# Performance work log

Measured on AMD Instinct MI355X. Metric: run time of the kernel, lower is better.

Reference implementation:

```python
import jax, jax.numpy as jnp
import numpy as np

N = 200_000   # nodes in batched graph
E = 400_000   # edges
D = 128       # embed_dim
L = 5         # num_layer
G = 1000      # number of graphs in batch
ATOM_V = 119  # atom vocab (OGB)
BOND_V = 5    # bond vocab (OGB)
OUT = 128     # output_dim
EPS = 1e-5


def setup_inputs() -> dict:
    key = jax.random.key(0)
    ks = jax.random.split(key, 16)
    inp = {
        "nfeat": jax.random.randint(ks[0], (N,), 0, ATOM_V),
        "efeat": jax.random.randint(ks[1], (E,), 0, BOND_V),
        "src": jax.random.randint(ks[2], (E,), 0, N),
        "dst": jax.random.randint(ks[3], (E,), 0, N),
        "node2graph": jnp.sort(jax.random.randint(ks[4], (N,), 0, G)),
        # learned parameters
        "atom_emb": jax.random.normal(ks[5], (ATOM_V, D), jnp.float32) * 0.02,
        "edge_emb": jax.random.normal(ks[6], (L, BOND_V, D), jnp.float32) * 0.02,
        "W": jax.random.normal(ks[7], (L, D, D), jnp.float32) * 0.02,
        "b": jnp.zeros((L, D), jnp.float32),
        "gamma": jnp.ones((L, D), jnp.float32),
        "beta": jnp.zeros((L, D), jnp.float32),
        "W1": jax.random.normal(ks[8], (D, D), jnp.float32) * 0.02,
        "b1": jnp.zeros((D,), jnp.float32),
        "W2": jax.random.normal(ks[9], (D, OUT), jnp.float32) * 0.02,
        "b2": jnp.zeros((OUT,), jnp.float32),
    }
    return inp


def reference(nfeat, efeat, src, dst, node2graph,
              atom_emb, edge_emb, W, b, gamma, beta, W1, b1, W2, b2):
    h = atom_emb[nfeat]                                  # [N, D]
    # in-degree + 1 (GCNConvLayer degree norm)
    deg = jax.ops.segment_sum(jnp.ones((E,), h.dtype), dst, num_segments=N) + 1.0
    for l in range(L):
        e = edge_emb[l][efeat]                           # [E, D] edge encoder
        m = h[src] + e                                   # u_add_e
        neigh = jax.ops.segment_sum(m, dst, num_segments=N)  # fn.sum -> 'neigh'
        h = ((h + neigh) / deg[:, None]) @ W[l] + b[l]   # project_node_feat
        # batch norm over nodes (training-mode batch stats), affine
        mu = jnp.mean(h, axis=0)
        var = jnp.var(h, axis=0)
        h = (h - mu) * jax.lax.rsqrt(var + EPS) * gamma[l] + beta[l]
        h = jax.nn.relu(h)                               # activation; dropout=eval
    # global mean pooling per graph
    cnt = jax.ops.segment_sum(jnp.ones((N,), h.dtype), node2graph, num_segments=G)
    g = jax.ops.segment_sum(h, node2graph, num_segments=G) / jnp.maximum(cnt, 1.0)[:, None]
    # predict MLP (dropout in eval mode = identity)
    out = jax.nn.relu(g @ W1 + b1) @ W2 + b2             # [G, OUT]
    return out
```

## Files before the change

kernel.cpp:

```cpp
#include <hip/hip_runtime.h>
#include <hip/hip_bf16.h>
#include <cstddef>

#define NN 200000
#define NE 400000
#define DD 128
#define NL 5
#define NG 1000
#define BOND_V 5
#define BM 32
#define NBLK (NN / BM)
#define MAXD 16
#define CHUNK 100
#define NB_SCAN 200
#define CH 1000
#define SB 125
#define EPS 1e-5f
#define XS 136

typedef __bf16 bf16x8 __attribute__((ext_vector_type(8)));
typedef float floatx4 __attribute__((ext_vector_type(4)));

__device__ __forceinline__ unsigned short f2bf(float f) {
    unsigned int u = __float_as_uint(f);
    u = (u + 0x7fffu + ((u >> 16) & 1u)) >> 16;
    return (unsigned short)u;
}
__device__ __forceinline__ float bf2f(unsigned short s) {
    return __uint_as_float(((unsigned int)s) << 16);
}
__device__ __forceinline__ float4 bf4_to_f4(uint2 v) {
    float4 o;
    o.x = __uint_as_float(v.x << 16);
    o.y = __uint_as_float(v.x & 0xffff0000u);
    o.z = __uint_as_float(v.y << 16);
    o.w = __uint_as_float(v.y & 0xffff0000u);
    return o;
}
__device__ __forceinline__ float4 actv4(float4 h, float4 sc, float4 sh) {
    float4 o;
    o.x = fmaxf(0.f, h.x * sc.x + sh.x);
    o.y = fmaxf(0.f, h.y * sc.y + sh.y);
    o.z = fmaxf(0.f, h.z * sc.z + sh.z);
    o.w = fmaxf(0.f, h.w * sc.w + sh.w);
    return o;
}

__global__ void k_setup1(const int* __restrict__ dst, int* __restrict__ cnt,
                         const int* __restrict__ n2g, float* __restrict__ gcnt,
                         const float* __restrict__ W, unsigned short* __restrict__ Wht,
                         unsigned short* __restrict__ Wlt) {
    int e = blockIdx.x * blockDim.x + threadIdx.x;
    if (e < NE) atomicAdd(&cnt[dst[e]], 1);
    if (e < NN) atomicAdd(&gcnt[n2g[e]], 1.0f);
    if (e < NL * DD * DD) {
        int l = e / (DD * DD), rem = e % (DD * DD);
        int k = rem / DD, n = rem % DD;
        float v = W[e];
        unsigned short hb = f2bf(v);
        unsigned short lb = f2bf(v - bf2f(hb));
        size_t o = (size_t)l * DD * DD + (size_t)n * DD + k;
        Wht[o] = hb; Wlt[o] = lb;
    }
}

__global__ void k_scan1(const int* __restrict__ cnt, int* __restrict__ bsum) {
    __shared__ int sh[256];
    int b = blockIdx.x, t = threadIdx.x;
    int s = 0;
    if (t < CH / 4) {
        int base = b * CH + t * 4;
        s = cnt[base] + cnt[base + 1] + cnt[base + 2] + cnt[base + 3];
    }
    sh[t] = s;
    __syncthreads();
    if (t == 0) {
        int tot = 0;
        for (int i = 0; i < CH / 4; i++) tot += sh[i];
        bsum[b] = tot;
    }
}

__global__ void k_scan2(const int* __restrict__ bsum, int* __restrict__ bpre,
                        int* __restrict__ off) {
    if (threadIdx.x == 0) {
        int run = 0;
        for (int i = 0; i < NB_SCAN; i++) { bpre[i] = run; run += bsum[i]; }
        off[NN] = NE;
    }
}

__global__ void k_scan3(const int* __restrict__ cnt, const int* __restrict__ bpre,
                        int* __restrict__ off, int* __restrict__ cur,
                        float* __restrict__ rdeg) {
    __shared__ int sh[256];
    int b = blockIdx.x, t = threadIdx.x;
    int base = b * CH + t * 4;
    int c0 = 0, c1 = 0, c2 = 0, c3 = 0, s = 0;
    if (t < CH / 4) {
        c0 = cnt[base]; c1 = cnt[base + 1]; c2 = cnt[base + 2]; c3 = cnt[base + 3];
        s = c0 + c1 + c2 + c3;
    }
    sh[t] = s;
    __syncthreads();
    if (t == 0) {
        int run = bpre[b];
        for (int i = 0; i < CH / 4; i++) { int v = sh[i]; sh[i] = run; run += v; }
    }
    __syncthreads();
    if (t < CH / 4) {
        int run = sh[t];
        off[base] = run; cur[base] = run; run += c0;
        off[base + 1] = run; cur[base + 1] = run; run += c1;
        off[base + 2] = run; cur[base + 2] = run; run += c2;
        off[base + 3] = run; cur[base + 3] = run;
        rdeg[base]     = 1.0f / (float)(c0 + 1);
        rdeg[base + 1] = 1.0f / (float)(c1 + 1);
        rdeg[base + 2] = 1.0f / (float)(c2 + 1);
        rdeg[base + 3] = 1.0f / (float)(c3 + 1);
    }
}

__global__ void k_bucket(const int* __restrict__ src, const int* __restrict__ dst,
                         const int* __restrict__ efeat, int* __restrict__ cur,
                         int* __restrict__ esrc, int* __restrict__ eft) {
    int e = blockIdx.x * blockDim.x + threadIdx.x;
    if (e < NE) {
        int p = atomicAdd(&cur[dst[e]], 1);
        esrc[p] = src[e];
        eft[p] = efeat[e];
    }
}

__global__ void k_pad(const int* __restrict__ off, const int* __restrict__ esrc,
                      const int* __restrict__ eft, const int* __restrict__ nfeat,
                      int* __restrict__ pent, int* __restrict__ pent0,
                      int* __restrict__ bperm, int* __restrict__ gmax) {
    __shared__ int offL[BM + 1];
    __shared__ int degS[BM];
    __shared__ int sortIdx[BM];
    __shared__ int gmaxS[8];
    int b = blockIdx.x, tid = threadIdx.x;
    if (tid <= BM) offL[tid] = off[b * BM + tid];
    __syncthreads();
    if (tid < BM) degS[tid] = offL[tid + 1] - offL[tid];
    __syncthreads();
    if (tid < BM) {
        int d = degS[tid], rank = 0;
        #pragma unroll
        for (int j = 0; j < BM; j++)
            rank += (degS[j] > d) || (degS[j] == d && j < tid);
        sortIdx[rank] = tid;
    }
    __syncthreads();
    if (tid < 8) {
        int g = degS[sortIdx[tid * 4]];
        gmaxS[tid] = g;
        gmax[b * 8 + tid] = g;
    }
    if (tid < BM) bperm[b * BM + tid] = sortIdx[tid];
    __syncthreads();
    for (int idx = tid; idx < BM * MAXD; idx += 256) {
        int p = idx & 31, j = idx >> 5, g = p >> 2;
        int gm = gmaxS[g]; if (gm > MAXD) gm = MAXD;
        if (j < gm) {
            int row = sortIdx[p];
            int d = degS[row];
            int v, v0;
            if (j < d) {
                int e = offL[row] + j;
                int s = esrc[e], f = eft[e];
                v = s | (f << 18);
                v0 = nfeat[s] | (f << 18);
            } else { v = (5 << 18); v0 = (5 << 18); }
            pent[(size_t)b * MAXD * BM + j * BM + p] = v;
            pent0[(size_t)b * MAXD * BM + j * BM + p] = v0;
        }
    }
}

__global__ __launch_bounds__(256, 4)
void k_fused(const void* __restrict__ basep, const int* __restrict__ nfeat, int first,
             const int* __restrict__ off, const int* __restrict__ esrc,
             const int* __restrict__ eft, const int* __restrict__ pentsel,
             const int* __restrict__ bperm, const int* __restrict__ gmax,
             const float* __restrict__ eemb, const float* __restrict__ rdeg,
             const float* __restrict__ scP, const float* __restrict__ shP,
             const unsigned short* __restrict__ Wht, const unsigned short* __restrict__ Wlt,
             const float* __restrict__ bias,
             unsigned short* __restrict__ C, float* __restrict__ part) {
    __shared__ unsigned short Xh[BM * XS];
    __shared__ unsigned short Xl[BM * XS];
    __shared__ float eSr[6 * DD];
    __shared__ int pentL[BM * MAXD];
    __shared__ int offL[BM + 1];
    __shared__ int permL[BM];
    __shared__ int gmL[8];

    const float* baseF = (const float*)basep;
    const unsigned short* baseB = (const unsigned short*)basep;

    int tid = threadIdx.x;
    int n0 = blockIdx.x * BM;
    if (tid < 160) *(float4*)(eSr + tid * 4) = *(const float4*)(eemb + tid * 4);
    else if (tid < 192) *(float4*)(eSr + tid * 4) = (float4){0.f, 0.f, 0.f, 0.f};
    if (tid <= BM) offL[tid] = off[n0 + tid];
    if (tid < BM) permL[tid] = bperm[blockIdx.x * BM + tid];
    if (tid < 8) gmL[tid] = gmax[blockIdx.x * 8 + tid];
    {
        const int2* pg = (const int2*)(pentsel + (size_t)blockIdx.x * MAXD * BM);
        *(int2*)(pentL + tid * 2) = pg[tid];
    }

    int lane32 = tid & 31, grp = tid >> 5;
    int c4 = lane32 << 2;
    float4 sc4, sh4;
    if (!first) {
        sc4 = *(const float4*)(scP + c4);
        sh4 = *(const float4*)(shP + c4);
    }
    __syncthreads();

    int rows[4];
    #pragma unroll
    for (int i = 0; i < 4; i++) rows[i] = permL[grp * 4 + i];

    float4 acc[4];
    #pragma unroll
    for (int i = 0; i < 4; i++) {
        int n = n0 + rows[i];
        if (first) {
            acc[i] = *(const float4*)(baseF + (size_t)nfeat[n] * DD + c4);
        } else {
            uint2 g = *(const uint2*)(baseB + (size_t)n * DD + c4);
            acc[i] = actv4(bf4_to_f4(g), sc4, sh4);
        }
    }

    int gmx = gmL[grp];
    int jmax = gmx < MAXD ? gmx : MAXD;
    const int* pL = pentL + grp * 4;
    int j = 0;
    if (first) {
        for (; j + 2 <= jmax; j += 2) {
            int a0 = pL[j*32+0], a1 = pL[j*32+1], a2 = pL[j*32+2], a3 = pL[j*32+3];
            int b0 = pL[j*32+32], b1 = pL[j*32+33], b2 = pL[j*32+34], b3 = pL[j*32+35];
            float4 ha0 = *(const float4*)(baseF + (size_t)(a0 & 0x3FFFF) * DD + c4);
            float4 ha1 = *(const float4*)(baseF + (size_t)(a1 & 0x3FFFF) * DD + c4);
            float4 ha2 = *(const float4*)(baseF + (size_t)(a2 & 0x3FFFF) * DD + c4);
            float4 ha3 = *(const float4*)(baseF + (size_t)(a3 & 0x3FFFF) * DD + c4);
            float4 hb0 = *(const float4*)(baseF + (size_t)(b0 & 0x3FFFF) * DD + c4);
            float4 hb1 = *(const float4*)(baseF + (size_t)(b1 & 0x3FFFF) * DD + c4);
            float4 hb2 = *(const float4*)(baseF + (size_t)(b2 & 0x3FFFF) * DD + c4);
            float4 hb3 = *(const float4*)(baseF + (size_t)(b3 & 0x3FFFF) * DD + c4);
            int fa0 = a0 >> 18, fa1 = a1 >> 18, fa2 = a2 >> 18, fa3 = a3 >> 18;
            int fb0 = b0 >> 18, fb1 = b1 >> 18, fb2 = b2 >> 18, fb3 = b3 >> 18;
            float wa0 = (fa0 == 5) ? 0.f : 1.f, wa1 = (fa1 == 5) ? 0.f : 1.f;
            float wa2 = (fa2 == 5) ? 0.f : 1.f, wa3 = (fa3 == 5) ? 0.f : 1.f;
            float wb0 = (fb0 == 5) ? 0.f : 1.f, wb1 = (fb1 == 5) ? 0.f : 1.f;
            float wb2 = (fb2 == 5) ? 0.f : 1.f, wb3 = (fb3 == 5) ? 0.f : 1.f;
            float4 ea0 = *(const float4*)(eSr + fa0 * DD + c4);
            float4 ea1 = *(const float4*)(eSr + fa1 * DD + c4);
            float4 ea2 = *(const float4*)(eSr + fa2 * DD + c4);
            float4 ea3 = *(const float4*)(eSr + fa3 * DD + c4);
            float4 eb0 = *(const float4*)(eSr + fb0 * DD + c4);
            float4 eb1 = *(const float4*)(eSr + fb1 * DD + c4);
            float4 eb2 = *(const float4*)(eSr + fb2 * DD + c4);
            float4 eb3 = *(const float4*)(eSr + fb3 * DD + c4);
            acc[0].x += (ha0.x + ea0.x) * wa0 + (hb0.x + eb0.x) * wb0;
            acc[0].y += (ha0.y + ea0.y) * wa0 + (hb0.y + eb0.y) * wb0;
            acc[0].z += (ha0.z + ea0.z) * wa0 + (hb0.z + eb0.z) * wb0;
            acc[0].w += (ha0.w + ea0.w) * wa0 + (hb0.w + eb0.w) * wb0;
            acc[1].x += (ha1.x + ea1.x) * wa1 + (hb1.x + eb1.x) * wb1;
            acc[1].y += (ha1.y + ea1.y) * wa1 + (hb1.y + eb1.y) * wb1;
            acc[1].z += (ha1.z + ea1.z) * wa1 + (hb1.z + eb1.z) * wb1;
            acc[1].w += (ha1.w + ea1.w) * wa1 + (hb1.w + eb1.w) * wb1;
            acc[2].x += (ha2.x + ea2.x) * wa2 + (hb2.x + eb2.x) * wb2;
            acc[2].y += (ha2.y + ea2.y) * wa2 + (hb2.y + eb2.y) * wb2;
            acc[2].z += (ha2.z + ea2.z) * wa2 + (hb2.z + eb2.z) * wb2;
            acc[2].w += (ha2.w + ea2.w) * wa2 + (hb2.w + eb2.w) * wb2;
            acc[3].x += (ha3.x + ea3.x) * wa3 + (hb3.x + eb3.x) * wb3;
            acc[3].y += (ha3.y + ea3.y) * wa3 + (hb3.y + eb3.y) * wb3;
            acc[3].z += (ha3.z + ea3.z) * wa3 + (hb3.z + eb3.z) * wb3;
            acc[3].w += (ha3.w + ea3.w) * wa3 + (hb3.w + eb3.w) * wb3;
        }
        for (; j < jmax; j++) {
            int a0 = pL[j*32+0], a1 = pL[j*32+1], a2 = pL[j*32+2], a3 = pL[j*32+3];
            float4 h0 = *(const float4*)(baseF + (size_t)(a0 & 0x3FFFF) * DD + c4);
            float4 h1 = *(const float4*)(baseF + (size_t)(a1 & 0x3FFFF) * DD + c4);
            float4 h2 = *(const float4*)(baseF + (size_t)(a2 & 0x3FFFF) * DD + c4);
            float4 h3 = *(const float4*)(baseF + (size_t)(a3 & 0x3FFFF) * DD + c4);
            int f0 = a0 >> 18, f1 = a1 >> 18, f2 = a2 >> 18, f3 = a3 >> 18;
            float w0 = (f0 == 5) ? 0.f : 1.f, w1 = (f1 == 5) ? 0.f : 1.f;
            float w2 = (f2 == 5) ? 0.f : 1.f, w3 = (f3 == 5) ? 0.f : 1.f;
            float4 e0 = *(const float4*)(eSr + f0 * DD + c4);
            float4 e1 = *(const float4*)(eSr + f1 * DD + c4);
            float4 e2 = *(const float4*)(eSr + f2 * DD + c4);
            float4 e3 = *(const float4*)(eSr + f3 * DD + c4);
            acc[0].x += (h0.x + e0.x) * w0; acc[0].y += (h0.y + e0.y) * w0;
            acc[0].z += (h0.z + e0.z) * w0; acc[0].w += (h0.w + e0.w) * w0;
            acc[1].x += (h1.x + e1.x) * w1; acc[1].y += (h1.y + e1.y) * w1;
            acc[1].z += (h1.z + e1.z) * w1; acc[1].w += (h1.w + e1.w) * w1;
            acc[2].x += (h2.x + e2.x) * w2; acc[2].y += (h2.y + e2.y) * w2;
            acc[2].z += (h2.z + e2.z) * w2; acc[2].w += (h2.w + e2.w) * w2;
            acc[3].x += (h3.x + e3.x) * w3; acc[3].y += (h3.y + e3.y) * w3;
            acc[3].z += (h3.z + e3.z) * w3; acc[3].w += (h3.w + e3.w) * w3;
        }
    } else {
        for (; j + 2 <= jmax; j += 2) {
            int a0 = pL[j*32+0], a1 = pL[j*32+1], a2 = pL[j*32+2], a3 = pL[j*32+3];
            int b0 = pL[j*32+32], b1 = pL[j*32+33], b2 = pL[j*32+34], b3 = pL[j*32+35];
            uint2 ga0 = *(const uint2*)(baseB + (size_t)(a0 & 0x3FFFF) * DD + c4);
            uint2 ga1 = *(const uint2*)(baseB + (size_t)(a1 & 0x3FFFF) * DD + c4);
            uint2 ga2 = *(const uint2*)(baseB + (size_t)(a2 & 0x3FFFF) * DD + c4);
            uint2 ga3 = *(const uint2*)(baseB + (size_t)(a3 & 0x3FFFF) * DD + c4);
            uint2 gb0 = *(const uint2*)(baseB + (size_t)(b0 & 0x3FFFF) * DD + c4);
            uint2 gb1 = *(const uint2*)(baseB + (size_t)(b1 & 0x3FFFF) * DD + c4);
            uint2 gb2 = *(const uint2*)(baseB + (size_t)(b2 & 0x3FFFF) * DD + c4);
            uint2 gb3 = *(const uint2*)(baseB + (size_t)(b3 & 0x3FFFF) * DD + c4);
            float4 ha0 = actv4(bf4_to_f4(ga0), sc4, sh4);
            float4 ha1 = actv4(bf4_to_f4(ga1), sc4, sh4);
            float4 ha2 = actv4(bf4_to_f4(ga2), sc4, sh4);
            float4 ha3 = actv4(bf4_to_f4(ga3), sc4, sh4);
            float4 hb0 = actv4(bf4_to_f4(gb0), sc4, sh4);
            float4 hb1 = actv4(bf4_to_f4(gb1), sc4, sh4);
            float4 hb2 = actv4(bf4_to_f4(gb2), sc4, sh4);
            float4 hb3 = actv4(bf4_to_f4(gb3), sc4, sh4);
            int fa0 = a0 >> 18, fa1 = a1 >> 18, fa2 = a2 >> 18, fa3 = a3 >> 18;
            int fb0 = b0 >> 18, fb1 = b1 >> 18, fb2 = b2 >> 18, fb3 = b3 >> 18;
            float wa0 = (fa0 == 5) ? 0.f : 1.f, wa1 = (fa1 == 5) ? 0.f : 1.f;
            float wa2 = (fa2 == 5) ? 0.f : 1.f, wa3 = (fa3 == 5) ? 0.f : 1.f;
            float wb0 = (fb0 == 5) ? 0.f : 1.f, wb1 = (fb1 == 5) ? 0.f : 1.f;
            float wb2 = (fb2 == 5) ? 0.f : 1.f, wb3 = (fb3 == 5) ? 0.f : 1.f;
            float4 ea0 = *(const float4*)(eSr + fa0 * DD + c4);
            float4 ea1 = *(const float4*)(eSr + fa1 * DD + c4);
            float4 ea2 = *(const float4*)(eSr + fa2 * DD + c4);
            float4 ea3 = *(const float4*)(eSr + fa3 * DD + c4);
            float4 eb0 = *(const float4*)(eSr + fb0 * DD + c4);
            float4 eb1 = *(const float4*)(eSr + fb1 * DD + c4);
            float4 eb2 = *(const float4*)(eSr + fb2 * DD + c4);
            float4 eb3 = *(const float4*)(eSr + fb3 * DD + c4);
            acc[0].x += (ha0.x + ea0.x) * wa0 + (hb0.x + eb0.x) * wb0;
            acc[0].y += (ha0.y + ea0.y) * wa0 + (hb0.y + eb0.y) * wb0;
            acc[0].z += (ha0.z + ea0.z) * wa0 + (hb0.z + eb0.z) * wb0;
            acc[0].w += (ha0.w + ea0.w) * wa0 + (hb0.w + eb0.w) * wb0;
            acc[1].x += (ha1.x + ea1.x) * wa1 + (hb1.x + eb1.x) * wb1;
            acc[1].y += (ha1.y + ea1.y) * wa1 + (hb1.y + eb1.y) * wb1;
            acc[1].z += (ha1.z + ea1.z) * wa1 + (hb1.z + eb1.z) * wb1;
            acc[1].w += (ha1.w + ea1.w) * wa1 + (hb1.w + eb1.w) * wb1;
            acc[2].x += (ha2.x + ea2.x) * wa2 + (hb2.x + eb2.x) * wb2;
            acc[2].y += (ha2.y + ea2.y) * wa2 + (hb2.y + eb2.y) * wb2;
            acc[2].z += (ha2.z + ea2.z) * wa2 + (hb2.z + eb2.z) * wb2;
            acc[2].w += (ha2.w + ea2.w) * wa2 + (hb2.w + eb2.w) * wb2;
            acc[3].x += (ha3.x + ea3.x) * wa3 + (hb3.x + eb3.x) * wb3;
            acc[3].y += (ha3.y + ea3.y) * wa3 + (hb3.y + eb3.y) * wb3;
            acc[3].z += (ha3.z + ea3.z) * wa3 + (hb3.z + eb3.z) * wb3;
            acc[3].w += (ha3.w + ea3.w) * wa3 + (hb3.w + eb3.w) * wb3;
        }
        for (; j < jmax; j++) {
            int a0 = pL[j*32+0], a1 = pL[j*32+1], a2 = pL[j*32+2], a3 = pL[j*32+3];
            uint2 g0 = *(const uint2*)(baseB + (size_t)(a0 & 0x3FFFF) * DD + c4);
            uint2 g1 = *(const uint2*)(baseB + (size_t)(a1 & 0x3FFFF) * DD + c4);
            uint2 g2 = *(const uint2*)(baseB + (size_t)(a2 & 0x3FFFF) * DD + c4);
            uint2 g3 = *(const uint2*)(baseB + (size_t)(a3 & 0x3FFFF) * DD + c4);
            float4 h0 = actv4(bf4_to_f4(g0), sc4, sh4);
            float4 h1 = actv4(bf4_to_f4(g1), sc4, sh4);
            float4 h2 = actv4(bf4_to_f4(g2), sc4, sh4);
            float4 h3 = actv4(bf4_to_f4(g3), sc4, sh4);
            int f0 = a0 >> 18, f1 = a1 >> 18, f2 = a2 >> 18, f3 = a3 >> 18;
            float w0 = (f0 == 5) ? 0.f : 1.f, w1 = (f1 == 5) ? 0.f : 1.f;
            float w2 = (f2 == 5) ? 0.f : 1.f, w3 = (f3 == 5) ? 0.f : 1.f;
            float4 e0 = *(const float4*)(eSr + f0 * DD + c4);
            float4 e1 = *(const float4*)(eSr + f1 * DD + c4);
            float4 e2 = *(const float4*)(eSr + f2 * DD + c4);
            float4 e3 = *(const float4*)(eSr + f3 * DD + c4);
            acc[0].x += (h0.x + e0.x) * w0; acc[0].y += (h0.y + e0.y) * w0;
            acc[0].z += (h0.z + e0.z) * w0; acc[0].w += (h0.w + e0.w) * w0;
            acc[1].x += (h1.x + e1.x) * w1; acc[1].y += (h1.y + e1.y) * w1;
            acc[1].z += (h1.z + e1.z) * w1; acc[1].w += (h1.w + e1.w) * w1;
            acc[2].x += (h2.x + e2.x) * w2; acc[2].y += (h2.y + e2.y) * w2;
            acc[2].z += (h2.z + e2.z) * w2; acc[2].w += (h2.w + e2.w) * w2;
            acc[3].x += (h3.x + e3.x) * w3; acc[3].y += (h3.y + e3.y) * w3;
            acc[3].z += (h3.z + e3.z) * w3; acc[3].w += (h3.w + e3.w) * w3;
        }
    }

    if (gmx > MAXD) {
        #pragma unroll
        for (int i = 0; i < 4; i++) {
            int row = rows[i];
            for (int e = offL[row] + MAXD; e < offL[row + 1]; e++) {
                int s = esrc[e], f = eft[e];
                float4 hv;
                if (first) {
                    hv = *(const float4*)(baseF + (size_t)nfeat[s] * DD + c4);
                } else {
                    uint2 g = *(const uint2*)(baseB + (size_t)s * DD + c4);
                    hv = actv4(bf4_to_f4(g), sc4, sh4);
                }
                const float* ep = eSr + f * DD + c4;
                acc[i].x += hv.x + ep[0]; acc[i].y += hv.y + ep[1];
                acc[i].z += hv.z + ep[2]; acc[i].w += hv.w + ep[3];
            }
        }
    }

    #pragma unroll
    for (int i = 0; i < 4; i++) {
        int r = rows[i];
        float rd = rdeg[n0 + r];
        float ax = acc[i].x * rd, ay = acc[i].y * rd, az = acc[i].z * rd, aw = acc[i].w * rd;
        unsigned short h0 = f2bf(ax), h1 = f2bf(ay), h2 = f2bf(az), h3 = f2bf(aw);
        unsigned short l0 = f2bf(ax - bf2f(h0));
        unsigned short l1 = f2bf(ay - bf2f(h1));
        unsigned short l2 = f2bf(az - bf2f(h2));
        unsigned short l3 = f2bf(aw - bf2f(h3));
        uint2 hv2, lv2;
        hv2.x = (unsigned)h0 | ((unsigned)h1 << 16);
        hv2.y = (unsigned)h2 | ((unsigned)h3 << 16);
        lv2.x = (unsigned)l0 | ((unsigned)l1 << 16);
        lv2.y = (unsigned)l2 | ((unsigned)l3 << 16);
        *(uint2*)(Xh + r * XS + c4) = hv2;
        *(uint2*)(Xl + r * XS + c4) = lv2;
    }
    __syncthreads();

    int lane = tid & 63, w = tid >> 6;
    int m16 = lane & 15, quad = lane >> 4;
    int rowTile = w & 1;
    int colBase = (w >> 1) << 6;
    int rowA = rowTile * 16 + m16;

    floatx4 acc4[4];
    #pragma unroll
    for (int t = 0; t < 4; t++) acc4[t] = (floatx4){0.f, 0.f, 0.f, 0.f};

    #pragma unroll
    for (int kp = 0; kp < 4; kp++) {
        bf16x8 ah = *(const bf16x8*)(Xh + rowA * XS + kp * 32 + quad * 8);
        bf16x8 al = *(const bf16x8*)(Xl + rowA * XS + kp * 32 + quad * 8);
        #pragma unroll
        for (int t = 0; t < 4; t++) {
            int ncol = colBase + t * 16 + m16;
            bf16x8 bh = *(const bf16x8*)(Wht + (size_t)ncol * DD + kp * 32 + quad * 8);
            bf16x8 bl = *(const bf16x8*)(Wlt + (size_t)ncol * DD + kp * 32 + quad * 8);
            acc4[t] = __builtin_amdgcn_mfma_f32_16x16x32_bf16(ah, bh, acc4[t], 0, 0, 0);
            acc4[t] = __builtin_amdgcn_mfma_f32_16x16x32_bf16(ah, bl, acc4[t], 0, 0, 0);
            acc4[t] = __builtin_amdgcn_mfma_f32_16x16x32_bf16(al, bh, acc4[t], 0, 0, 0);
        }
    }
    __syncthreads();

    float* redS = eSr;
    float* redQ = eSr + 2 * DD;
    unsigned short* Cs = Xh;
    #pragma unroll
    for (int t = 0; t < 4; t++) {
        int col = colBase + t * 16 + m16;
        float bv = bias[col];
        float s = 0.f, q = 0.f;
        #pragma unroll
        for (int rr = 0; rr < 4; rr++) {
            float vv = acc4[t][rr] + bv;
            s += vv; q += vv * vv;
            Cs[(rowTile * 16 + quad * 4 + rr) * XS + col] = f2bf(vv);
        }
        s += __shfl_xor(s, 16); q += __shfl_xor(q, 16);
        s += __shfl_xor(s, 32); q += __shfl_xor(q, 32);
        if (lane < 16) { redS[rowTile * DD + col] = s; redQ[rowTile * DD + col] = q; }
    }
    __syncthreads();

    #pragma unroll
    for (int it = 0; it < 2; it++) {
        int idx = it * 256 + tid;
        int row = idx >> 4, q16 = idx & 15;
        uint4 v = *(const uint4*)(Cs + row * XS + q16 * 8);
        *(uint4*)(C + (size_t)(n0 + row) * DD + q16 * 8) = v;
    }
    if (tid < DD) {
        float ss = redS[tid] + redS[DD + tid];
        float qq = redQ[tid] + redQ[DD + tid];
        part[(size_t)blockIdx.x * 256 + tid] = ss;
        part[(size_t)blockIdx.x * 256 + DD + tid] = qq;
    }
}

__global__ void k_stats(const float* __restrict__ part, float* __restrict__ acc,
                        int* __restrict__ cnt,
                        const float* __restrict__ gamma, const float* __restrict__ beta,
                        float* __restrict__ scale, float* __restrict__ shift) {
    int t = threadIdx.x;
    float s = 0.f;
    int base = blockIdx.x * (NBLK / SB);
    for (int i = 0; i < NBLK / SB; i++)
        s += part[(size_t)(base + i) * 256 + t];
    atomicAdd(&acc[t], s);
    __threadfence();
    __shared__ int lastS;
    __syncthreads();
    if (t == 0) lastS = (atomicAdd(cnt, 1) == SB - 1);
    __syncthreads();
    if (lastS && t < DD) {
        float Sv = atomicAdd(&acc[t], 0.0f);
        float Qv = atomicAdd(&acc[DD + t], 0.0f);
        float m = Sv / (float)NN;
        float v = Qv / (float)NN - m * m;
        float rs = rsqrtf(v + EPS);
        float sc = rs * gamma[t];
        scale[t] = sc;
        shift[t] = beta[t] - m * sc;
    }
}

__global__ void k_bnpool(const unsigned short* __restrict__ A, const int* __restrict__ n2g,
                         const float* __restrict__ scale, const float* __restrict__ shift,
                         float* __restrict__ gsum) {
    int j = threadIdx.x;
    int n0 = blockIdx.x * CHUNK;
    float sc = scale[j], sh = shift[j];
    int cur = n2g[n0];
    float acc = 0.f;
    for (int i = 0; i < CHUNK; i++) {
        int n = n0 + i;
        int gg = n2g[n];
        if (gg != cur) {
            atomicAdd(&gsum[(size_t)cur * DD + j], acc);
            acc = 0.f;
            cur = gg;
        }
        float x = bf2f(A[(size_t)n * DD + j]);
        acc += fmaxf(0.f, x * sc + sh);
    }
    atomicAdd(&gsum[(size_t)cur * DD + j], acc);
}

__global__ void k_mlp(const float* __restrict__ gsum, const float* __restrict__ gcnt,
                      const float* __restrict__ W1, const float* __restrict__ b1,
                      const float* __restrict__ W2, const float* __restrict__ b2,
                      float* __restrict__ out) {
    __shared__ float gs[DD], hs[DD];
    int gid = blockIdx.x, j = threadIdx.x;
    float inv = 1.0f / fmaxf(gcnt[gid], 1.0f);
    gs[j] = gsum[(size_t)gid * DD + j] * inv;
    __syncthreads();
    float a = b1[j];
    for (int k = 0; k < DD; k++) a += gs[k] * W1[k * DD + j];
    hs[j] = fmaxf(a, 0.f);
    __syncthreads();
    float o = b2[j];
    for (int k = 0; k < DD; k++) o += hs[k] * W2[k * DD + j];
    out[(size_t)gid * DD + j] = o;
}

extern "C" void kernel_launch(void* const* d_in, const int* in_sizes, int n_in,
                              void* d_out, int out_size, void* d_ws, size_t ws_size,
                              hipStream_t stream) {
    const int*   nfeat = (const int*)d_in[0];
    const int*   efeat = (const int*)d_in[1];
    const int*   src   = (const int*)d_in[2];
    const int*   dst   = (const int*)d_in[3];
    const int*   n2g   = (const int*)d_in[4];
    const float* aemb  = (const float*)d_in[5];
    const float* eemb  = (const float*)d_in[6];
    const float* Wl    = (const float*)d_in[7];
    const float* bl    = (const float*)d_in[8];
    const float* gam   = (const float*)d_in[9];
    const float* bet   = (const float*)d_in[10];
    const float* W1    = (const float*)d_in[11];
    const float* b1    = (const float*)d_in[12];
    const float* W2    = (const float*)d_in[13];
    const float* b2    = (const float*)d_in[14];
    float* out = (float*)d_out;

    unsigned short* H0 = (unsigned short*)d_ws;
    unsigned short* H1 = H0 + (size_t)NN * DD;
    float* rdeg   = (float*)(H1 + (size_t)NN * DD);
    float* gsum   = rdeg + NN;
    float* gcnt   = gsum + (size_t)NG * DD;
    float* scaleA = gcnt + NG;
    float* shiftA = scaleA + NL * DD;
    float* accS   = shiftA + NL * DD;
    int*   scnt   = (int*)(accS + NL * 256);
    float* part   = (float*)(scnt + 16);
    unsigned short* Wht = (unsigned short*)(part + (size_t)NBLK * 256);
    unsigned short* Wlt = Wht + (size_t)NL * DD * DD;
    int* off   = (int*)(Wlt + (size_t)NL * DD * DD);
    int* cur   = off + NN + 1;
    int* esrc  = cur + NN;
    int* eft   = esrc + NE;
    int* cnt   = eft + NE;
    int* bsum  = cnt + NN;
    int* bpre  = bsum + NB_SCAN;
    int* bperm = bpre + NB_SCAN;
    int* gmax  = bperm + (size_t)NBLK * BM;
    int* pent  = gmax + (size_t)NBLK * 8;
    int* pent0 = pent + (size_t)NBLK * MAXD * BM;

    hipMemsetAsync(gsum, 0, (size_t)(NG * DD + NG) * sizeof(float), stream);
    hipMemsetAsync(accS, 0, (size_t)(NL * 256) * sizeof(float) + 16 * sizeof(int), stream);
    hipMemsetAsync(cnt, 0, (size_t)NN * sizeof(int), stream);

    k_setup1<<<(NE + 255) / 256, 256, 0, stream>>>(dst, cnt, n2g, gcnt, Wl, Wht, Wlt);
    k_scan1<<<NB_SCAN, 256, 0, stream>>>(cnt, bsum);
    k_scan2<<<1, 64, 0, stream>>>(bsum, bpre, off);
    k_scan3<<<NB_SCAN, 256, 0, stream>>>(cnt, bpre, off, cur, rdeg);
    k_bucket<<<(NE + 255) / 256, 256, 0, stream>>>(src, dst, efeat, cur, esrc, eft);
    k_pad<<<NBLK, 256, 0, stream>>>(off, esrc, eft, nfeat, pent, pent0, bperm, gmax);

    unsigned short* hcur = H0;
    for (int l = 0; l < NL; l++) {
        const void* base = (l == 0) ? (const void*)aemb : (const void*)hcur;
        unsigned short* hnext = (l == 0) ? H0 : ((hcur == H0) ? H1 : H0);
        const int* psel = (l == 0) ? pent0 : pent;
        const float* scP = scaleA + (size_t)((l == 0) ? 0 : (l - 1)) * DD;
        const float* shP = shiftA + (size_t)((l == 0) ? 0 : (l - 1)) * DD;
        k_fused<<<NBLK, 256, 0, stream>>>(base, nfeat, (l == 0) ? 1 : 0,
                                          off, esrc, eft, psel, bperm, gmax,
                                          eemb + (size_t)l * BOND_V * DD, rdeg,
                                          scP, shP,
                                          Wht + (size_t)l * DD * DD,
                                          Wlt + (size_t)l * DD * DD,
                                          bl + (size_t)l * DD, hnext, part);
        k_stats<<<SB, 256, 0, stream>>>(part, accS + l * 256, scnt + l,
                                        gam + (size_t)l * DD, bet + (size_t)l * DD,
                                        scaleA + (size_t)l * DD, shiftA + (size_t)l * DD);
        hcur = hnext;
    }
    k_bnpool<<<NN / CHUNK, DD, 0, stream>>>(hcur, n2g,
                                            scaleA + (size_t)(NL - 1) * DD,
                                            shiftA + (size_t)(NL - 1) * DD, gsum);
    k_mlp<<<NG, DD, 0, stream>>>(gsum, gcnt, W1, b1, W2, b2, out);
}
```

Measured before the change: 1.036 ms.

## Software-pipeline neighbor gathers, drop smem metadata, vectorize pooling kernel

In the layered aggregation kernel, the non-first path now prefetches the next edge slot's neighbor rows while accumulating the current ones (unroll-1 double buffer). Per-block metadata (perm, gmax, offsets) is read straight from global memory instead of staged through shared memory, and the barrier is moved after the self-row loads. k_pad always fills all MAXD padded slots so the kernel can round the trip count up to even without a remainder loop. Launch bounds are raised to 6 waves per EU, and the pooling kernel uses 256 threads with bf16x4 vector loads over 8 node stripes. The cost is extra padded iterations, possible register pressure at the higher occupancy target, and more atomics in pooling.

```diff
diff --git a/kernel.cpp b/kernel.cpp
--- a/kernel.cpp
+++ b/kernel.cpp
@@ -11,7 +11,7 @@
 #define BM 32
 #define NBLK (NN / BM)
 #define MAXD 16
-#define CHUNK 100
+#define PCH 200
 #define NB_SCAN 200
 #define CH 1000
 #define SB 125
@@ -139,7 +139,6 @@
     __shared__ int offL[BM + 1];
     __shared__ int degS[BM];
     __shared__ int sortIdx[BM];
-    __shared__ int gmaxS[8];
     int b = blockIdx.x, tid = threadIdx.x;
     if (tid <= BM) offL[tid] = off[b * BM + tid];
     __syncthreads();
@@ -153,33 +152,26 @@
         sortIdx[rank] = tid;
     }
     __syncthreads();
-    if (tid < 8) {
-        int g = degS[sortIdx[tid * 4]];
-        gmaxS[tid] = g;
-        gmax[b * 8 + tid] = g;
-    }
+    if (tid < 8) gmax[b * 8 + tid] = degS[sortIdx[tid * 4]];
     if (tid < BM) bperm[b * BM + tid] = sortIdx[tid];
     __syncthreads();
     for (int idx = tid; idx < BM * MAXD; idx += 256) {
-        int p = idx & 31, j = idx >> 5, g = p >> 2;
-        int gm = gmaxS[g]; if (gm > MAXD) gm = MAXD;
-        if (j < gm) {
-            int row = sortIdx[p];
-            int d = degS[row];
-            int v, v0;
-            if (j < d) {
-                int e = offL[row] + j;
-                int s = esrc[e], f = eft[e];
-                v = s | (f << 18);
-                v0 = nfeat[s] | (f << 18);
-            } else { v = (5 << 18); v0 = (5 << 18); }
-            pent[(size_t)b * MAXD * BM + j * BM + p] = v;
-            pent0[(size_t)b * MAXD * BM + j * BM + p] = v0;
-        }
-    }
-}
-
-__global__ __launch_bounds__(256, 4)
+        int p = idx & 31, j = idx >> 5;
+        int row = sortIdx[p];
+        int d = degS[row];
+        int v, v0;
+        if (j < d) {
+            int e = offL[row] + j;
+            int s = esrc[e], f = eft[e];
+            v = s | (f << 18);
+            v0 = nfeat[s] | (f << 18);
+        } else { v = (5 << 18); v0 = (5 << 18); }
+        pent[(size_t)b * MAXD * BM + j * BM + p] = v;
+        pent0[(size_t)b * MAXD * BM + j * BM + p] = v0;
+    }
+}
+
+__global__ __launch_bounds__(256, 6)
 void k_fused(const void* __restrict__ basep, const int* __restrict__ nfeat, int first,
              const int* __restrict__ off, const int* __restrict__ esrc,
              const int* __restrict__ eft, const int* __restrict__ pentsel,
@@ -193,9 +185,6 @@
     __shared__ unsigned short Xl[BM * XS];
     __shared__ float eSr[6 * DD];
     __shared__ int pentL[BM * MAXD];
-    __shared__ int offL[BM + 1];
-    __shared__ int permL[BM];
-    __shared__ int gmL[8];
 
     const float* baseF = (const float*)basep;
     const unsigned short* baseB = (const unsigned short*)basep;
@@ -204,9 +193,6 @@
     int n0 = blockIdx.x * BM;
     if (tid < 160) *(float4*)(eSr + tid * 4) = *(const float4*)(eemb + tid * 4);
     else if (tid < 192) *(float4*)(eSr + tid * 4) = (float4){0.f, 0.f, 0.f, 0.f};
-    if (tid <= BM) offL[tid] = off[n0 + tid];
-    if (tid < BM) permL[tid] = bperm[blockIdx.x * BM + tid];
-    if (tid < 8) gmL[tid] = gmax[blockIdx.x * 8 + tid];
     {
         const int2* pg = (const int2*)(pentsel + (size_t)blockIdx.x * MAXD * BM);
         *(int2*)(pentL + tid * 2) = pg[tid];
@@ -219,11 +205,11 @@
         sc4 = *(const float4*)(scP + c4);
         sh4 = *(const float4*)(shP + c4);
     }
-    __syncthreads();
 
     int rows[4];
     #pragma unroll
-    for (int i = 0; i < 4; i++) rows[i] = permL[grp * 4 + i];
+    for (int i = 0; i < 4; i++) rows[i] = bperm[blockIdx.x * BM + grp * 4 + i];
+    int gmx = gmax[blockIdx.x * 8 + grp];
 
     float4 acc[4];
     #pragma unroll
@@ -236,13 +222,14 @@
             acc[i] = actv4(bf4_to_f4(g), sc4, sh4);
         }
     }
-
-    int gmx = gmL[grp];
-    int jmax = gmx < MAXD ? gmx : MAXD;
+    __syncthreads();
+
+    int jE = gmx < MAXD ? gmx : MAXD;
+    jE = (jE + 1) & ~1;
     const int* pL = pentL + grp * 4;
-    int j = 0;
+
     if (first) {
-        for (; j + 2 <= jmax; j += 2) {
+        for (int j = 0; j < jE; j += 2) {
             int a0 = pL[j*32+0], a1 = pL[j*32+1], a2 = pL[j*32+2], a3 = pL[j*32+3];
             int b0 = pL[j*32+32], b1 = pL[j*32+33], b2 = pL[j*32+34], b3 = pL[j*32+35];
             float4 ha0 = *(const float4*)(baseF + (size_t)(a0 & 0x3FFFF) * DD + c4);
@@ -284,104 +271,68 @@
             acc[3].z += (ha3.z + ea3.z) * wa3 + (hb3.z + eb3.z) * wb3;
             acc[3].w += (ha3.w + ea3.w) * wa3 + (hb3.w + eb3.w) * wb3;
         }
-        for (; j < jmax; j++) {
-            int a0 = pL[j*32+0], a1 = pL[j*32+1], a2 = pL[j*32+2], a3 = pL[j*32+3];
-            float4 h0 = *(const float4*)(baseF + (size_t)(a0 & 0x3FFFF) * DD + c4);
-            float4 h1 = *(const float4*)(baseF + (size_t)(a1 & 0x3FFFF) * DD + c4);
-            float4 h2 = *(const float4*)(baseF + (size_t)(a2 & 0x3FFFF) * DD + c4);
-            float4 h3 = *(const float4*)(baseF + (size_t)(a3 & 0x3FFFF) * DD + c4);
-            int f0 = a0 >> 18, f1 = a1 >> 18, f2 = a2 >> 18, f3 = a3 >> 18;
-            float w0 = (f0 == 5) ? 0.f : 1.f, w1 = (f1 == 5) ? 0.f : 1.f;
-            float w2 = (f2 == 5) ? 0.f : 1.f, w3 = (f3 == 5) ? 0.f : 1.f;
-            float4 e0 = *(const float4*)(eSr + f0 * DD + c4);
-            float4 e1 = *(const float4*)(eSr + f1 * DD + c4);
-            float4 e2 = *(const float4*)(eSr + f2 * DD + c4);
-            float4 e3 = *(const float4*)(eSr + f3 * DD + c4);
-            acc[0].x += (h0.x + e0.x) * w0; acc[0].y += (h0.y + e0.y) * w0;
-            acc[0].z += (h0.z + e0.z) * w0; acc[0].w += (h0.w + e0.w) * w0;
-            acc[1].x += (h1.x + e1.x) * w1; acc[1].y += (h1.y + e1.y) * w1;
-            acc[1].z += (h1.z + e1.z) * w1; acc[1].w += (h1.w + e1.w) * w1;
-            acc[2].x += (h2.x + e2.x) * w2; acc[2].y += (h2.y + e2.y) * w2;
-            acc[2].z += (h2.z + e2.z) * w2; acc[2].w += (h2.w + e2.w) * w2;
-            acc[3].x += (h3.x + e3.x) * w3; acc[3].y += (h3.y + e3.y) * w3;
-            acc[3].z += (h3.z + e3.z) * w3; acc[3].w += (h3.w + e3.w) * w3;
-        }
     } else {
-        for (; j + 2 <= jmax; j += 2) {
-            int a0 = pL[j*32+0], a1 = pL[j*32+1], a2 = pL[j*32+2], a3 = pL[j*32+3];
-            int b0 = pL[j*32+32], b1 = pL[j*32+33], b2 = pL[j*32+34], b3 = pL[j*32+35];
-            uint2 ga0 = *(const uint2*)(baseB + (size_t)(a0 & 0x3FFFF) * DD + c4);
-            uint2 ga1 = *(const uint2*)(baseB + (size_t)(a1 & 0x3FFFF) * DD + c4);
-            uint2 ga2 = *(const uint2*)(baseB + (size_t)(a2 & 0x3FFFF) * DD + c4);
-            uint2 ga3 = *(const uint2*)(baseB + (size_t)(a3 & 0x3FFFF) * DD + c4);
-            uint2 gb0 = *(const uint2*)(baseB + (size_t)(b0 & 0x3FFFF) * DD + c4);
-            uint2 gb1 = *(const uint2*)(baseB + (size_t)(b1 & 0x3FFFF) * DD + c4);
-            uint2 gb2 = *(const uint2*)(baseB + (size_t)(b2 & 0x3FFFF) * DD + c4);
-            uint2 gb3 = *(const uint2*)(baseB + (size_t)(b3 & 0x3FFFF) * DD + c4);
-            float4 ha0 = actv4(bf4_to_f4(ga0), sc4, sh4);
-            float4 ha1 = actv4(bf4_to_f4(ga1), sc4, sh4);
-            float4 ha2 = actv4(bf4_to_f4(ga2), sc4, sh4);
-            float4 ha3 = actv4(bf4_to_f4(ga3), sc4, sh4);
-            float4 hb0 = actv4(bf4_to_f4(gb0), sc4, sh4);
-            float4 hb1 = actv4(bf4_to_f4(gb1), sc4, sh4);
-            float4 hb2 = actv4(bf4_to_f4(gb2), sc4, sh4);
-            float4 hb3 = actv4(bf4_to_f4(gb3), sc4, sh4);
-            int fa0 = a0 >> 18, fa1 = a1 >> 18, fa2 = a2 >> 18, fa3 = a3 >> 18;
-            int fb0 = b0 >> 18, fb1 = b1 >> 18, fb2 = b2 >> 18, fb3 = b3 >> 18;
-            float wa0 = (fa0 == 5) ? 0.f : 1.f, wa1 = (fa1 == 5) ? 0.f : 1.f;
-            float wa2 = (fa2 == 5) ? 0.f : 1.f, wa3 = (fa3 == 5) ? 0.f : 1.f;
-            float wb0 = (fb0 == 5) ? 0.f : 1.f, wb1 = (fb1 == 5) ? 0.f : 1.f;
-            float wb2 = (fb2 == 5) ? 0.f : 1.f, wb3 = (fb3 == 5) ? 0.f : 1.f;
-            float4 ea0 = *(const float4*)(eSr + fa0 * DD + c4);
-            float4 ea1 = *(const float4*)(eSr + fa1 * DD + c4);
-            float4 ea2 = *(const float4*)(eSr + fa2 * DD + c4);
-            float4 ea3 = *(const float4*)(eSr + fa3 * DD + c4);
-            float4 eb0 = *(const float4*)(eSr + fb0 * DD + c4);
-            float4 eb1 = *(const float4*)(eSr + fb1 * DD + c4);
-            float4 eb2 = *(const float4*)(eSr + fb2 * DD + c4);
-            float4 eb3 = *(const float4*)(eSr + fb3 * DD + c4);
-            acc[0].x += (ha0.x + ea0.x) * wa0 + (hb0.x + eb0.x) * wb0;
-            acc[0].y += (ha0.y + ea0.y) * wa0 + (hb0.y + eb0.y) * wb0;
-            acc[0].z += (ha0.z + ea0.z) * wa0 + (hb0.z + eb0.z) * wb0;
-            acc[0].w += (ha0.w + ea0.w) * wa0 + (hb0.w + eb0.w) * wb0;
-            acc[1].x += (ha1.x + ea1.x) * wa1 + (hb1.x + eb1.x) * wb1;
-            acc[1].y += (ha1.y + ea1.y) * wa1 + (hb1.y + eb1.y) * wb1;
-            acc[1].z += (ha1.z + ea1.z) * wa1 + (hb1.z + eb1.z) * wb1;
-            acc[1].w += (ha1.w + ea1.w) * wa1 + (hb1.w + eb1.w) * wb1;
-            acc[2].x += (ha2.x + ea2.x) * wa2 + (hb2.x + eb2.x) * wb2;
-            acc[2].y += (ha2.y + ea2.y) * wa2 + (hb2.y + eb2.y) * wb2;
-            acc[2].z += (ha2.z + ea2.z) * wa2 + (hb2.z + eb2.z) * wb2;
-            acc[2].w += (ha2.w + ea2.w) * wa2 + (hb2.w + eb2.w) * wb2;
-            acc[3].x += (ha3.x + ea3.x) * wa3 + (hb3.x + eb3.x) * wb3;
-            acc[3].y += (ha3.y + ea3.y) * wa3 + (hb3.y + eb3.y) * wb3;
-            acc[3].z += (ha3.z + ea3.z) * wa3 + (hb3.z + eb3.z) * wb3;
-            acc[3].w += (ha3.w + ea3.w) * wa3 + (hb3.w + eb3.w) * wb3;
-        }
-        for (; j < jmax; j++) {
-            int a0 = pL[j*32+0], a1 = pL[j*32+1], a2 = pL[j*32+2], a3 = pL[j*32+3];
-            uint2 g0 = *(const uint2*)(baseB + (size_t)(a0 & 0x3FFFF) * DD + c4);
-            uint2 g1 = *(const uint2*)(baseB + (size_t)(a1 & 0x3FFFF) * DD + c4);
-            uint2 g2 = *(const uint2*)(baseB + (size_t)(a2 & 0x3FFFF) * DD + c4);
-            uint2 g3 = *(const uint2*)(baseB + (size_t)(a3 & 0x3FFFF) * DD + c4);
-            float4 h0 = actv4(bf4_to_f4(g0), sc4, sh4);
-            float4 h1 = actv4(bf4_to_f4(g1), sc4, sh4);
-            float4 h2 = actv4(bf4_to_f4(g2), sc4, sh4);
-            float4 h3 = actv4(bf4_to_f4(g3), sc4, sh4);
-            int f0 = a0 >> 18, f1 = a1 >> 18, f2 = a2 >> 18, f3 = a3 >> 18;
-            float w0 = (f0 == 5) ? 0.f : 1.f, w1 = (f1 == 5) ? 0.f : 1.f;
-            float w2 = (f2 == 5) ? 0.f : 1.f, w3 = (f3 == 5) ? 0.f : 1.f;
-            float4 e0 = *(const float4*)(eSr + f0 * DD + c4);
-            float4 e1 = *(const float4*)(eSr + f1 * DD + c4);
-            float4 e2 = *(const float4*)(eSr + f2 * DD + c4);
-            float4 e3 = *(const float4*)(eSr + f3 * DD + c4);
-            acc[0].x += (h0.x + e0.x) * w0; acc[0].y += (h0.y + e0.y) * w0;
-            acc[0].z += (h0.z + e0.z) * w0; acc[0].w += (h0.w + e0.w) * w0;
-            acc[1].x += (h1.x + e1.x) * w1; acc[1].y += (h1.y + e1.y) * w1;
-            acc[1].z += (h1.z + e1.z) * w1; acc[1].w += (h1.w + e1.w) * w1;
-            acc[2].x += (h2.x + e2.x) * w2; acc[2].y += (h2.y + e2.y) * w2;
-            acc[2].z += (h2.z + e2.z) * w2; acc[2].w += (h2.w + e2.w) * w2;
-            acc[3].x += (h3.x + e3.x) * w3; acc[3].y += (h3.y + e3.y) * w3;
-            acc[3].z += (h3.z + e3.z) * w3; acc[3].w += (h3.w + e3.w) * w3;
+        int pa0 = pL[0], pa1 = pL[1], pa2 = pL[2], pa3 = pL[3];
+        uint2 ga0 = *(const uint2*)(baseB + (size_t)(pa0 & 0x3FFFF) * DD + c4);
+        uint2 ga1 = *(const uint2*)(baseB + (size_t)(pa1 & 0x3FFFF) * DD + c4);
+        uint2 ga2 = *(const uint2*)(baseB + (size_t)(pa2 & 0x3FFFF) * DD + c4);
+        uint2 ga3 = *(const uint2*)(baseB + (size_t)(pa3 & 0x3FFFF) * DD + c4);
+        #pragma unroll 1
+        for (int j = 0; j < jE; j += 2) {
+            int pb0 = pL[(j+1)*32+0], pb1 = pL[(j+1)*32+1];
+            int pb2 = pL[(j+1)*32+2], pb3 = pL[(j+1)*32+3];
+            uint2 gb0 = *(const uint2*)(baseB + (size_t)(pb0 & 0x3FFFF) * DD + c4);
+            uint2 gb1 = *(const uint2*)(baseB + (size_t)(pb1 & 0x3FFFF) * DD + c4);
+            uint2 gb2 = *(const uint2*)(baseB + (size_t)(pb2 & 0x3FFFF) * DD + c4);
+            uint2 gb3 = *(const uint2*)(baseB + (size_t)(pb3 & 0x3FFFF) * DD + c4);
+            {
+                float4 h0 = actv4(bf4_to_f4(ga0), sc4, sh4);
+                float4 h1 = actv4(bf4_to_f4(ga1), sc4, sh4);
+                float4 h2 = actv4(bf4_to_f4(ga2), sc4, sh4);
+                float4 h3 = actv4(bf4_to_f4(ga3), sc4, sh4);
+                int f0 = pa0 >> 18, f1 = pa1 >> 18, f2 = pa2 >> 18, f3 = pa3 >> 18;
+                float w0 = (f0 == 5) ? 0.f : 1.f, w1 = (f1 == 5) ? 0.f : 1.f;
+                float w2 = (f2 == 5) ? 0.f : 1.f, w3 = (f3 == 5) ? 0.f : 1.f;
+                float4 e0 = *(const float4*)(eSr + f0 * DD + c4);
+                float4 e1 = *(const float4*)(eSr + f1 * DD + c4);
+                float4 e2 = *(const float4*)(eSr + f2 * DD + c4);
+                float4 e3 = *(const float4*)(eSr + f3 * DD + c4);
+                acc[0].x += (h0.x + e0.x) * w0; acc[0].y += (h0.y + e0.y) * w0;
+                acc[0].z += (h0.z + e0.z) * w0; acc[0].w += (h0.w + e0.w) * w0;
+                acc[1].x += (h1.x + e1.x) * w1; acc[1].y += (h1.y + e1.y) * w1;
+                acc[1].z += (h1.z + e1.z) * w1; acc[1].w += (h1.w + e1.w) * w1;
+                acc[2].x += (h2.x + e2.x) * w2; acc[2].y += (h2.y + e2.y) * w2;
+                acc[2].z += (h2.z + e2.z) * w2; acc[2].w += (h2.w + e2.w) * w2;
+                acc[3].x += (h3.x + e3.x) * w3; acc[3].y += (h3.y + e3.y) * w3;
+                acc[3].z += (h3.z + e3.z) * w3; acc[3].w += (h3.w + e3.w) * w3;
+            }
+            int j2 = (j + 2 < MAXD) ? (j + 2) : (MAXD - 1);
+            pa0 = pL[j2*32+0]; pa1 = pL[j2*32+1]; pa2 = pL[j2*32+2]; pa3 = pL[j2*32+3];
+            ga0 = *(const uint2*)(baseB + (size_t)(pa0 & 0x3FFFF) * DD + c4);
+            ga1 = *(const uint2*)(baseB + (size_t)(pa1 & 0x3FFFF) * DD + c4);
+            ga2 = *(const uint2*)(baseB + (size_t)(pa2 & 0x3FFFF) * DD + c4);
+            ga3 = *(const uint2*)(baseB + (size_t)(pa3 & 0x3FFFF) * DD + c4);
+            {
+                float4 h0 = actv4(bf4_to_f4(gb0), sc4, sh4);
+                float4 h1 = actv4(bf4_to_f4(gb1), sc4, sh4);
+                float4 h2 = actv4(bf4_to_f4(gb2), sc4, sh4);
+                float4 h3 = actv4(bf4_to_f4(gb3), sc4, sh4);
+                int f0 = pb0 >> 18, f1 = pb1 >> 18, f2 = pb2 >> 18, f3 = pb3 >> 18;
+                float w0 = (f0 == 5) ? 0.f : 1.f, w1 = (f1 == 5) ? 0.f : 1.f;
+                float w2 = (f2 == 5) ? 0.f : 1.f, w3 = (f3 == 5) ? 0.f : 1.f;
+                float4 e0 = *(const float4*)(eSr + f0 * DD + c4);
+                float4 e1 = *(const float4*)(eSr + f1 * DD + c4);
+                float4 e2 = *(const float4*)(eSr + f2 * DD + c4);
+                float4 e3 = *(const float4*)(eSr + f3 * DD + c4);
+                acc[0].x += (h0.x + e0.x) * w0; acc[0].y += (h0.y + e0.y) * w0;
+                acc[0].z += (h0.z + e0.z) * w0; acc[0].w += (h0.w + e0.w) * w0;
+                acc[1].x += (h1.x + e1.x) * w1; acc[1].y += (h1.y + e1.y) * w1;
+                acc[1].z += (h1.z + e1.z) * w1; acc[1].w += (h1.w + e1.w) * w1;
+                acc[2].x += (h2.x + e2.x) * w2; acc[2].y += (h2.y + e2.y) * w2;
+                acc[2].z += (h2.z + e2.z) * w2; acc[2].w += (h2.w + e2.w) * w2;
+                acc[3].x += (h3.x + e3.x) * w3; acc[3].y += (h3.y + e3.y) * w3;
+                acc[3].z += (h3.z + e3.z) * w3; acc[3].w += (h3.w + e3.w) * w3;
+            }
         }
     }
 
@@ -389,7 +340,8 @@
         #pragma unroll
         for (int i = 0; i < 4; i++) {
             int row = rows[i];
-            for (int e = offL[row] + MAXD; e < offL[row + 1]; e++) {
+            int e0 = off[n0 + row] + MAXD, e1 = off[n0 + row + 1];
+            for (int e = e0; e < e1; e++) {
                 int s = esrc[e], f = eft[e];
                 float4 hv;
                 if (first) {
@@ -516,23 +468,36 @@
 __global__ void k_bnpool(const unsigned short* __restrict__ A, const int* __restrict__ n2g,
                          const float* __restrict__ scale, const float* __restrict__ shift,
                          float* __restrict__ gsum) {
-    int j = threadIdx.x;
-    int n0 = blockIdx.x * CHUNK;
-    float sc = scale[j], sh = shift[j];
-    int cur = n2g[n0];
-    float acc = 0.f;
-    for (int i = 0; i < CHUNK; i++) {
-        int n = n0 + i;
+    int tid = threadIdx.x;
+    int stripe = tid >> 5, lane = tid & 31;
+    int c4 = lane << 2;
+    int n0 = blockIdx.x * PCH;
+    float4 sc4 = *(const float4*)(scale + c4);
+    float4 sh4 = *(const float4*)(shift + c4);
+    float4 acc = {0.f, 0.f, 0.f, 0.f};
+    int cur = n2g[n0 + stripe];
+    for (int i = 0; i < PCH / 8; i++) {
+        int n = n0 + i * 8 + stripe;
         int gg = n2g[n];
         if (gg != cur) {
-            atomicAdd(&gsum[(size_t)cur * DD + j], acc);
-            acc = 0.f;
+            atomicAdd(&gsum[(size_t)cur * DD + c4 + 0], acc.x);
+            atomicAdd(&gsum[(size_t)cur * DD + c4 + 1], acc.y);
+            atomicAdd(&gsum[(size_t)cur * DD + c4 + 2], acc.z);
+            atomicAdd(&gsum[(size_t)cur * DD + c4 + 3], acc.w);
+            acc = (float4){0.f, 0.f, 0.f, 0.f};
             cur = gg;
         }
-        float x = bf2f(A[(size_t)n * DD + j]);
-        acc += fmaxf(0.f, x * sc + sh);
-    }
-    atomicAdd(&gsum[(size_t)cur * DD + j], acc);
+        uint2 v = *(const uint2*)(A + (size_t)n * DD + c4);
+        float4 x = bf4_to_f4(v);
+        acc.x += fmaxf(0.f, x.x * sc4.x + sh4.x);
+        acc.y += fmaxf(0.f, x.y * sc4.y + sh4.y);
+        acc.z += fmaxf(0.f, x.z * sc4.z + sh4.z);
+        acc.w += fmaxf(0.f, x.w * sc4.w + sh4.w);
+    }
+    atomicAdd(&gsum[(size_t)cur * DD + c4 + 0], acc.x);
+    atomicAdd(&gsum[(size_t)cur * DD + c4 + 1], acc.y);
+    atomicAdd(&gsum[(size_t)cur * DD + c4 + 2], acc.z);
+    atomicAdd(&gsum[(size_t)cur * DD + c4 + 3], acc.w);
 }
 
 __global__ void k_mlp(const float* __restrict__ gsum, const float* __restrict__ gcnt,
@@ -627,8 +592,8 @@
                                         scaleA + (size_t)l * DD, shiftA + (size_t)l * DD);
         hcur = hnext;
     }
-    k_bnpool<<<NN / CHUNK, DD, 0, stream>>>(hcur, n2g,
-                                            scaleA + (size_t)(NL - 1) * DD,
-                                            shiftA + (size_t)(NL - 1) * DD, gsum);
+    k_bnpool<<<NN / PCH, 256, 0, stream>>>(hcur, n2g,
+                                           scaleA + (size_t)(NL - 1) * DD,
+                                           shiftA + (size_t)(NL - 1) * DD, gsum);
     k_mlp<<<NG, DD, 0, stream>>>(gsum, gcnt, W1, b1, W2, b2, out);
 }
```

Measured after the change: 1.221 ms. +17.8%, slower.
